# Kernel tuning notes

Hardware: AMD Instinct MI355X
Metric: run time of the kernel (lower is better)

The kernel has to match this reference:

```python
import jax, jax.numpy as jnp
import numpy as np

B, N, D = 2, 2048, 1024
CTX, TV = 256, 250
H, DH = 16, 64
INNER = H * DH          # 1024
FF = 4 * D              # 4096 (GEGLU inner)
SCALE = DH ** -0.5


def _layernorm(x, g, b):
    mu = x.mean(-1, keepdims=True)
    var = ((x - mu) ** 2).mean(-1, keepdims=True)
    return (x - mu) / jnp.sqrt(var + 1e-5) * g + b


def _attn(xq, ctx, wq, wk, wv, wo, bo):
    b, n, _ = xq.shape
    m = ctx.shape[1]
    q = (xq @ wq).reshape(b, n, H, DH)
    k = (ctx @ wk).reshape(b, m, H, DH)
    v = (ctx @ wv).reshape(b, m, H, DH)
    sim = jnp.einsum('bihd,bjhd->bhij', q, k) * SCALE
    att = jax.nn.softmax(sim, axis=-1)
    out = jnp.einsum('bhij,bjhd->bihd', att, v).reshape(b, n, INNER)
    return out @ wo + bo


def _sin_pe(T, d):
    pos = jnp.arange(T, dtype=jnp.float32)[:, None]
    den = jnp.power(10000.0, 2.0 * jnp.arange(d // 2, dtype=jnp.float32) / d)
    ang = pos / den                                  # [T, d/2]
    return jnp.stack([jnp.sin(ang), jnp.cos(ang)], -1).reshape(T, d)


def setup_inputs() -> dict:
    key = jax.random.key(0)
    ks = jax.random.split(key, 40)
    w = lambda k, s: jax.random.normal(k, s, jnp.float32) * 0.02
    inp = {
        'x': jax.random.normal(ks[0], (B, N, D), jnp.float32),
        'context': jax.random.normal(ks[1], (B, CTX, D), jnp.float32),
        'hint_control': jax.random.normal(ks[2], (B, TV, D), jnp.float32),
        'ln1_g': jnp.ones((D,)), 'ln1_b': jnp.zeros((D,)),
        'ln2_g': jnp.ones((D,)), 'ln2_b': jnp.zeros((D,)),
        'ln3_g': jnp.ones((D,)), 'ln3_b': jnp.zeros((D,)),
        'ln4_g': jnp.ones((D,)), 'ln4_b': jnp.zeros((D,)),
        'a1_wq': w(ks[3], (D, INNER)), 'a1_wk': w(ks[4], (D, INNER)),
        'a1_wv': w(ks[5], (D, INNER)), 'a1_wo': w(ks[6], (INNER, D)),
        'a1_bo': jnp.zeros((D,)),
        'a2_wq': w(ks[7], (D, INNER)), 'a2_wk': w(ks[8], (D, INNER)),
        'a2_wv': w(ks[9], (D, INNER)), 'a2_wo': w(ks[10], (INNER, D)),
        'a2_bo': jnp.zeros((D,)),
        'a3_wq': w(ks[11], (D, INNER)), 'a3_wk': w(ks[12], (D, INNER)),
        'a3_wv': w(ks[13], (D, INNER)), 'a3_wo': w(ks[14], (INNER, D)),
        'a3_bo': jnp.zeros((D,)),
        'ff_w1': w(ks[15], (D, 2 * FF)), 'ff_b1': jnp.zeros((2 * FF,)),
        'ff_w2': w(ks[16], (FF, D)), 'ff_b2': jnp.zeros((D,)),
    }
    return inp


def reference(x, context, hint_control,
              ln1_g, ln1_b, ln2_g, ln2_b, ln3_g, ln3_b, ln4_g, ln4_b,
              a1_wq, a1_wk, a1_wv, a1_wo, a1_bo,
              a2_wq, a2_wk, a2_wv, a2_wo, a2_bo,
              a3_wq, a3_wk, a3_wv, a3_wo, a3_bo,
              ff_w1, ff_b1, ff_w2, ff_b2):
    # attn1: self-attention (disable_self_attn=False -> context is x itself)
    h = _layernorm(x, ln1_g, ln1_b)
    x = _attn(h, h, a1_wq, a1_wk, a1_wv, a1_wo, a1_bo) + x
    # attn2: cross-attention over context
    h = _layernorm(x, ln2_g, ln2_b)
    x = _attn(h, context, a2_wq, a2_wk, a2_wv, a2_wo, a2_bo) + x
    # attn3: video cross-attention with sinusoidal PE added to hint_control
    hint = hint_control + _sin_pe(hint_control.shape[1], D)[None]
    h = _layernorm(x, ln4_g, ln4_b)
    x = _attn(h, hint, a3_wq, a3_wk, a3_wv, a3_wo, a3_bo) + x
    # GEGLU feed-forward
    h = _layernorm(x, ln3_g, ln3_b)
    proj = h @ ff_w1 + ff_b1
    a, gate = jnp.split(proj, 2, axis=-1)
    x = (a * jax.nn.gelu(gate, approximate=False)) @ ff_w2 + ff_b2 + x
    return x
```

## Files before the change

### kernel.cpp

```cpp
#include <hip/hip_runtime.h>
#include <cstdint>

typedef unsigned short u16;
typedef __bf16 bf16x8 __attribute__((ext_vector_type(8)));
typedef float f32x4 __attribute__((ext_vector_type(4)));

__device__ __forceinline__ u16 f2bf(float f) {
  union { float f; uint32_t u; } x; x.f = f;
  uint32_t r = x.u + 0x7FFFu + ((x.u >> 16) & 1u);
  return (u16)(r >> 16);
}
__device__ __forceinline__ bf16x8 ld8s(const u16* p) {
  return *reinterpret_cast<const bf16x8*>(p);
}
__device__ __forceinline__ float geluf(float x) {
  return 0.5f * x * (1.f + erff(x * 0.70710678118654752f));
}
__device__ __forceinline__ uint32_t cvtpk(float a, float b) {
  uint32_t r;
  asm("v_cvt_pk_bf16_f32 %0, %1, %2" : "=v"(r) : "v"(a), "v"(b));
  return r;
}
__device__ __forceinline__ void gload16(const u16* g, u16* l) {
  __builtin_amdgcn_global_load_lds(
      (__attribute__((address_space(1))) void*)const_cast<u16*>(g),
      (__attribute__((address_space(3))) void*)l, 16, 0, 0);
}

struct PrepJob {
  const void* src; void* dst;
  int K, N, mode, row_off, ldo, s_lo, s_hi, blk0;
};
struct PrepArgs { PrepJob j[17]; };

__global__ __launch_bounds__(256) void wprep_kernel(PrepArgs a) {
  __shared__ float tile[32][33];
  int bid = blockIdx.x;
  int t = threadIdx.x;
  const float* src = nullptr; void* dst = nullptr;
  int K = 0, N = 0, mode = 0, roff = 0, ldo = 0, slo = 0, shi = 0, bl = 0;
#pragma unroll
  for (int i = 0; i < 17; ++i) {
    int lo = a.j[i].blk0;
    int hi = (i == 16) ? 0x7fffffff : a.j[i + 1].blk0;
    if (bid >= lo && bid < hi) {
      src = (const float*)a.j[i].src; dst = a.j[i].dst;
      K = a.j[i].K; N = a.j[i].N; mode = a.j[i].mode; roff = a.j[i].row_off;
      ldo = a.j[i].ldo; slo = a.j[i].s_lo; shi = a.j[i].s_hi; bl = bid - lo;
    }
  }
  (void)K;
  if (mode <= 1) {
    int nb = N >> 5;
    int bx = bl % nb, by = bl / nb;
    int tx = t & 31, ty = t >> 5;
    int n = bx * 32 + tx, kbase = by * 32;
#pragma unroll
    for (int r = 0; r < 4; ++r)
      tile[ty + r * 8][tx] = src[(size_t)(kbase + ty + r * 8) * N + n];
    __syncthreads();
#pragma unroll
    for (int r = 0; r < 4; ++r) {
      int nl = ty + r * 8, ng = bx * 32 + nl;
      int orow;
      if (mode == 0) orow = roff + ng;
      else {
        if (ng < 4096) orow = ((ng >> 4) << 5) + (ng & 15);
        else { int t2 = ng - 4096; orow = ((t2 >> 4) << 5) + 16 + (t2 & 15); }
      }
      float v = tile[tx][nl];
      if (mode == 0 && orow >= slo && orow < shi) v *= 0.18033688011112042f;
      ((u16*)dst)[(size_t)orow * ldo + kbase + tx] = f2bf(v);
    }
  } else if (mode == 2) {
    int idx = bl * 1024 + t * 4;
    float4 v = *reinterpret_cast<const float4*>(src + idx);
    ushort4 o;
    o.x = f2bf(v.x); o.y = f2bf(v.y); o.z = f2bf(v.z); o.w = f2bf(v.w);
    *reinterpret_cast<ushort4*>((u16*)dst + idx) = o;
  } else if (mode == 3) {
    int row = bl;
    int tt = row % 250;
    int d0 = t * 4;
    int i0 = d0 >> 1;
    float den0 = powf(10000.f, (float)i0 / 512.f);
    float den1 = powf(10000.f, (float)(i0 + 1) / 512.f);
    float a0 = (float)tt / den0, a1 = (float)tt / den1;
    const float* hp = src + (size_t)row * 1024 + d0;
    u16* op = (u16*)dst + (size_t)row * 1024 + d0;
    op[0] = f2bf(hp[0] + sinf(a0));
    op[1] = f2bf(hp[1] + cosf(a0));
    op[2] = f2bf(hp[2] + sinf(a1));
    op[3] = f2bf(hp[3] + cosf(a1));
  } else {
    int i2 = bl * 256 + t;
    int g = i2 >> 5, s2 = i2 & 31;
    int c2 = (s2 < 16) ? (g * 16 + s2) : (4096 + g * 16 + (s2 - 16));
    ((float*)dst)[i2] = src[c2];
  }
}

__global__ __launch_bounds__(256) void ln_kernel(const float* __restrict__ x,
                                                 const float* __restrict__ g,
                                                 const float* __restrict__ b,
                                                 u16* __restrict__ out) {
  int row = blockIdx.x;
  int tid = threadIdx.x;
  int l = tid & 63, w = tid >> 6;
  const float4 v = reinterpret_cast<const float4*>(x + (size_t)row * 1024)[tid];
  float s = v.x + v.y + v.z + v.w;
#pragma unroll
  for (int d = 1; d < 64; d <<= 1) s += __shfl_xor(s, d, 64);
  __shared__ float red[8];
  if (l == 0) red[w] = s;
  __syncthreads();
  float mean = (red[0] + red[1] + red[2] + red[3]) * (1.f / 1024.f);
  float dx = v.x - mean, dy = v.y - mean, dz = v.z - mean, dw = v.w - mean;
  float vs = dx * dx + dy * dy + dz * dz + dw * dw;
#pragma unroll
  for (int d = 1; d < 64; d <<= 1) vs += __shfl_xor(vs, d, 64);
  if (l == 0) red[4 + w] = vs;
  __syncthreads();
  float var = (red[4] + red[5] + red[6] + red[7]) * (1.f / 1024.f);
  float rstd = rsqrtf(var + 1e-5f);
  const float4 g4 = reinterpret_cast<const float4*>(g)[tid];
  const float4 b4 = reinterpret_cast<const float4*>(b)[tid];
  ushort4 o;
  o.x = f2bf(dx * rstd * g4.x + b4.x);
  o.y = f2bf(dy * rstd * g4.y + b4.y);
  o.z = f2bf(dz * rstd * g4.z + b4.z);
  o.w = f2bf(dw * rstd * g4.w + b4.w);
  reinterpret_cast<ushort4*>(out + (size_t)row * 1024)[tid] = o;
}

template <int EPI>
__global__ __launch_bounds__(512, 2) void gemm256_kernel(
    const u16* __restrict__ A, int lda, const u16* __restrict__ Bt,
    void* __restrict__ Cv, int ldc, const float* __restrict__ bias,
    int M, int N, int K) {
  __shared__ __align__(16) u16 As[2][256 * 64];
  __shared__ __align__(16) u16 Bs[2][256 * 64];
  int t = threadIdx.x;
  int l = t & 63, w = t >> 6;
  int wm = w >> 2, wn = w & 3;
  int lr = l & 15, lg = l >> 4;
  int gx = gridDim.x;
  int nwg = gx * gridDim.y;
  int orig = blockIdx.y * gx + blockIdx.x;
  int qq = nwg >> 3, rr = nwg & 7;
  int xcd = orig & 7, lin = orig >> 3;
  int wg = (xcd < rr ? xcd * (qq + 1) : rr * (qq + 1) + (xcd - rr) * qq) + lin;
  int bx = wg % gx, by = wg / gx;
  int row0 = by * 256, n0 = bx * 256;

  int lrow8 = l >> 3, lchunk = l & 7;
  int csrc = (lchunk ^ lrow8) * 8;
  int keyA = lr & 7;

  f32x4 acc[8][4];
#pragma unroll
  for (int i = 0; i < 8; ++i)
#pragma unroll
    for (int j = 0; j < 4; ++j) acc[i][j] = f32x4{0.f, 0.f, 0.f, 0.f};

  auto stage = [&](int buf, int k0) {
#pragma unroll
    for (int q = 0; q < 4; ++q) {
      int rbase = w * 32 + q * 8;
      int r = rbase + lrow8;
      gload16(&A[(size_t)(row0 + r) * lda + k0 + csrc], &As[buf][rbase * 64]);
      gload16(&Bt[(size_t)(n0 + r) * K + k0 + csrc], &Bs[buf][rbase * 64]);
    }
  };

  int nk = K >> 6;
  stage(0, 0);
  if (nk > 1) {
    stage(1, 64);
    asm volatile("s_waitcnt vmcnt(8)" ::: "memory");
  } else {
    asm volatile("s_waitcnt vmcnt(0)" ::: "memory");
  }
  __builtin_amdgcn_sched_barrier(0);
  __builtin_amdgcn_s_barrier();
  int cur = 0;
  for (int ti = 0; ti < nk; ++ti) {
    __builtin_amdgcn_s_setprio(1);
#pragma unroll
    for (int kk = 0; kk < 2; ++kk) {
      int chunk = (((kk << 2) + lg) ^ keyA) << 3;
      bf16x8 af[8];
#pragma unroll
      for (int mi = 0; mi < 8; ++mi)
        af[mi] = ld8s(&As[cur][(wm * 128 + mi * 16 + lr) * 64 + chunk]);
      bf16x8 bfv[4];
#pragma unroll
      for (int ni = 0; ni < 4; ++ni)
        bfv[ni] = ld8s(&Bs[cur][(wn * 64 + ni * 16 + lr) * 64 + chunk]);
#pragma unroll
      for (int mi = 0; mi < 8; ++mi)
#pragma unroll
        for (int ni = 0; ni < 4; ++ni)
          acc[mi][ni] = __builtin_amdgcn_mfma_f32_16x16x32_bf16(af[mi], bfv[ni], acc[mi][ni], 0, 0, 0);
    }
    __builtin_amdgcn_s_setprio(0);
    __builtin_amdgcn_sched_barrier(0);
    __builtin_amdgcn_s_barrier();
    if (ti + 2 < nk) {
      stage(cur, (ti + 2) << 6);
      asm volatile("s_waitcnt vmcnt(8)" ::: "memory");
    } else {
      asm volatile("s_waitcnt vmcnt(0)" ::: "memory");
    }
    __builtin_amdgcn_sched_barrier(0);
    __builtin_amdgcn_s_barrier();
    cur ^= 1;
  }

#pragma unroll
  for (int mi = 0; mi < 8; ++mi) {
    int rowb = row0 + wm * 128 + mi * 16 + lg * 4;
    if (EPI == 2) {
#pragma unroll
      for (int p = 0; p < 2; ++p) {
        int colA = n0 + wn * 64 + p * 32 + lr;
        int colG = colA + 16;
        int ocol = ((n0 + wn * 64) >> 1) + p * 16 + lr;
#pragma unroll
        for (int r = 0; r < 4; ++r) {
          float av = acc[mi][2 * p][r] + bias[colA];
          float gv = acc[mi][2 * p + 1][r] + bias[colG];
          ((u16*)Cv)[(size_t)(rowb + r) * ldc + ocol] = f2bf(av * geluf(gv));
        }
      }
    } else {
#pragma unroll
      for (int ni = 0; ni < 4; ++ni) {
        int gcol = n0 + wn * 64 + ni * 16 + lr;
#pragma unroll
        for (int r = 0; r < 4; ++r)
          ((u16*)Cv)[(size_t)(rowb + r) * ldc + gcol] = f2bf(acc[mi][ni][r]);
      }
    }
  }
}

template <int EPI, bool GUARD>
__global__ __launch_bounds__(256) void gemm_bt_kernel(
    const u16* __restrict__ A, int lda, const u16* __restrict__ Bt,
    void* __restrict__ Cv, int ldc, const float* __restrict__ bias,
    const float* __restrict__ res, int M, int N, int K) {
  __shared__ __align__(16) u16 As[2][128 * 64];
  __shared__ __align__(16) u16 Bs[2][128 * 64];
  int t = threadIdx.x;
  int l = t & 63, w = t >> 6;
  int wm = w >> 1, wn = w & 1;
  int lr = l & 15, lg = l >> 4;
  int gx = gridDim.x;
  int nwg = gx * gridDim.y;
  int orig = blockIdx.y * gx + blockIdx.x;
  int qq = nwg >> 3, rr = nwg & 7;
  int xcd = orig & 7, lin = orig >> 3;
  int wg = (xcd < rr ? xcd * (qq + 1) : rr * (qq + 1) + (xcd - rr) * qq) + lin;
  int bx = wg % gx, by = wg / gx;
  int row0 = by * 128, n0 = bx * 128;

  int lrow8 = l >> 3, lchunk = l & 7;
  int csrc = (lchunk ^ lrow8) * 8;
  int keyA = lr & 7;
  f32x4 acc[4][4];
#pragma unroll
  for (int i = 0; i < 4; ++i)
#pragma unroll
    for (int j = 0; j < 4; ++j) acc[i][j] = f32x4{0.f, 0.f, 0.f, 0.f};

  auto stage = [&](int buf, int k0) {
#pragma unroll
    for (int q = 0; q < 4; ++q) {
      int rbase = w * 32 + q * 8;
      int r = rbase + lrow8;
      int ga = row0 + r;
      if (GUARD) { if (ga > M - 1) ga = M - 1; }
      gload16(&A[(size_t)ga * lda + k0 + csrc], &As[buf][rbase * 64]);
      gload16(&Bt[(size_t)(n0 + r) * K + k0 + csrc], &Bs[buf][rbase * 64]);
    }
  };

  int nk = K >> 6;
  stage(0, 0);
  if (nk > 1) {
    stage(1, 64);
    asm volatile("s_waitcnt vmcnt(8)" ::: "memory");
  } else {
    asm volatile("s_waitcnt vmcnt(0)" ::: "memory");
  }
  __builtin_amdgcn_sched_barrier(0);
  __builtin_amdgcn_s_barrier();
  int cur = 0;
  for (int ti = 0; ti < nk; ++ti) {
    __builtin_amdgcn_s_setprio(1);
#pragma unroll
    for (int kk = 0; kk < 2; ++kk) {
      bf16x8 af[4], bfv[4];
#pragma unroll
      for (int mi = 0; mi < 4; ++mi)
        af[mi] = ld8s(&As[cur][(wm * 64 + mi * 16 + lr) * 64 + ((((kk << 2) + lg) ^ keyA) << 3)]);
#pragma unroll
      for (int ni = 0; ni < 4; ++ni)
        bfv[ni] = ld8s(&Bs[cur][(wn * 64 + ni * 16 + lr) * 64 + ((((kk << 2) + lg) ^ keyA) << 3)]);
#pragma unroll
      for (int mi = 0; mi < 4; ++mi)
#pragma unroll
        for (int ni = 0; ni < 4; ++ni)
          acc[mi][ni] = __builtin_amdgcn_mfma_f32_16x16x32_bf16(af[mi], bfv[ni], acc[mi][ni], 0, 0, 0);
    }
    __builtin_amdgcn_s_setprio(0);
    __builtin_amdgcn_sched_barrier(0);
    __builtin_amdgcn_s_barrier();
    if (ti + 2 < nk) {
      stage(cur, (ti + 2) << 6);
      asm volatile("s_waitcnt vmcnt(8)" ::: "memory");
    } else {
      asm volatile("s_waitcnt vmcnt(0)" ::: "memory");
    }
    __builtin_amdgcn_sched_barrier(0);
    __builtin_amdgcn_s_barrier();
    cur ^= 1;
  }

#pragma unroll
  for (int mi = 0; mi < 4; ++mi) {
    int rowb = row0 + wm * 64 + mi * 16 + lg * 4;
    if (EPI == 2) {
#pragma unroll
      for (int p = 0; p < 2; ++p) {
        int colA = n0 + wn * 64 + p * 32 + lr;
        int colG = colA + 16;
        int ocol = ((n0 + wn * 64) >> 1) + p * 16 + lr;
#pragma unroll
        for (int r = 0; r < 4; ++r) {
          int grow = rowb + r;
          float av = acc[mi][2 * p][r] + bias[colA];
          float gv = acc[mi][2 * p + 1][r] + bias[colG];
          ((u16*)Cv)[(size_t)grow * ldc + ocol] = f2bf(av * geluf(gv));
        }
      }
    } else {
#pragma unroll
      for (int ni = 0; ni < 4; ++ni) {
        int gcol = n0 + wn * 64 + ni * 16 + lr;
#pragma unroll
        for (int r = 0; r < 4; ++r) {
          int grow = rowb + r;
          if (GUARD && grow >= M) continue;
          float v = acc[mi][ni][r];
          if (EPI == 0)
            ((u16*)Cv)[(size_t)grow * ldc + gcol] = f2bf(v);
          else
            ((float*)Cv)[(size_t)grow * ldc + gcol] =
                v + bias[gcol] + res[(size_t)grow * ldc + gcol];
        }
      }
    }
  }
}

template <bool TG>
__global__ __launch_bounds__(256) void attn_kernel(
    const u16* __restrict__ Q, int qs, int qoff,
    const u16* __restrict__ KV, int kvs, int koff, int voff,
    int m, u16* __restrict__ O) {
  int b = blockIdx.z, h = blockIdx.y;
  int t = threadIdx.x;
  int l = t & 63, w = t >> 6;
  int lr = l & 15, lg = l >> 4;
  int q0 = blockIdx.x * 128 + w * 16;
  __shared__ __align__(16) u16 Ks[2][64 * 64];
  __shared__ __align__(16) u16 Vt[2][64 * 64];
  __shared__ __align__(16) u16 Pl[4][16 * 64];

  const u16* qrowA = Q + (size_t)((b << 11) + q0 + lr) * qs + qoff + h * 64;
  const u16* qrowB = qrowA + (size_t)64 * qs;
  bf16x8 qa0 = ld8s(qrowA + lg * 8), qa1 = ld8s(qrowA + 32 + lg * 8);
  bf16x8 qb0 = ld8s(qrowB + lg * 8), qb1 = ld8s(qrowB + 32 + lg * 8);

  f32x4 oA[4], oB[4];
  float psA = 0.f, psB = 0.f;
#pragma unroll
  for (int r = 0; r < 4; ++r) { oA[r] = f32x4{0.f, 0.f, 0.f, 0.f}; oB[r] = f32x4{0.f, 0.f, 0.f, 0.f}; }

  const u16* kvb = KV + (size_t)b * m * kvs + h * 64;
  int kj = t >> 3, kc = t & 7;
  int srcsw = ((l & 7) ^ (l >> 3)) << 3;
  int psw = (lr & 7) ^ ((lr & 8) >> 1);

  {
#pragma unroll
    for (int q2 = 0; q2 < 2; ++q2) {
      int gr = w * 16 + q2 * 8 + (l >> 3);
      if (TG) { if (gr > m - 1) gr = m - 1; }
      gload16(kvb + (size_t)gr * kvs + koff + srcsw, &Ks[0][(w * 16 + q2 * 8) * 64]);
    }
    int jv = kj * 2;
    int gv0 = jv, gv1 = jv + 1;
    if (TG) { if (gv0 > m - 1) gv0 = m - 1; if (gv1 > m - 1) gv1 = m - 1; }
    uint4 va = *reinterpret_cast<const uint4*>(kvb + (size_t)gv0 * kvs + voff + kc * 8);
    uint4 vb2 = *reinterpret_cast<const uint4*>(kvb + (size_t)gv1 * kvs + voff + kc * 8);
    const u16* vap = reinterpret_cast<const u16*>(&va);
    const u16* vbp = reinterpret_cast<const u16*>(&vb2);
    int jb = jv >> 3, jlow = jv & 7;
#pragma unroll
    for (int i = 0; i < 8; ++i) {
      int d = kc * 8 + i;
      int key = (d ^ (d >> 3)) & 7;
      uint32_t pk = (uint32_t)vap[i] | ((uint32_t)vbp[i] << 16);
      *reinterpret_cast<uint32_t*>(&Vt[0][d * 64 + ((jb ^ key) << 3) + jlow]) = pk;
    }
  }
  __syncthreads();

  int nj = (m + 63) >> 6;
  int cur = 0;
  for (int jt = 0; jt < nj; ++jt) {
    int j0 = jt << 6;
    bool hn = (jt + 1 < nj);
    uint4 va, vb2;
    if (hn) {
      int j0n = j0 + 64;
#pragma unroll
      for (int q2 = 0; q2 < 2; ++q2) {
        int gr = j0n + w * 16 + q2 * 8 + (l >> 3);
        if (TG) { if (gr > m - 1) gr = m - 1; }
        gload16(kvb + (size_t)gr * kvs + koff + srcsw, &Ks[cur ^ 1][(w * 16 + q2 * 8) * 64]);
      }
      int jv = kj * 2;
      int gv0 = j0n + jv, gv1 = j0n + jv + 1;
      if (TG) { if (gv0 > m - 1) gv0 = m - 1; if (gv1 > m - 1) gv1 = m - 1; }
      va = *reinterpret_cast<const uint4*>(kvb + (size_t)gv0 * kvs + voff + kc * 8);
      vb2 = *reinterpret_cast<const uint4*>(kvb + (size_t)gv1 * kvs + voff + kc * 8);
    }

    const u16* Kb = Ks[cur];
    f32x4 sA[4], sB[4];
#pragma unroll
    for (int c = 0; c < 4; ++c) {
      sA[c] = f32x4{0.f, 0.f, 0.f, 0.f};
      sB[c] = f32x4{0.f, 0.f, 0.f, 0.f};
      bf16x8 k0 = ld8s(&Kb[(c * 16 + lr) * 64 + ((lg ^ (lr & 7)) << 3)]);
      bf16x8 k1 = ld8s(&Kb[(c * 16 + lr) * 64 + (((4 + lg) ^ (lr & 7)) << 3)]);
      sA[c] = __builtin_amdgcn_mfma_f32_16x16x32_bf16(k0, qa0, sA[c], 0, 0, 0);
      sA[c] = __builtin_amdgcn_mfma_f32_16x16x32_bf16(k1, qa1, sA[c], 0, 0, 0);
      sB[c] = __builtin_amdgcn_mfma_f32_16x16x32_bf16(k0, qb0, sB[c], 0, 0, 0);
      sB[c] = __builtin_amdgcn_mfma_f32_16x16x32_bf16(k1, qb1, sB[c], 0, 0, 0);
    }

    if (hn) {
      const u16* vap = reinterpret_cast<const u16*>(&va);
      const u16* vbp = reinterpret_cast<const u16*>(&vb2);
      int jv = kj * 2;
      int jb = jv >> 3, jlow = jv & 7;
#pragma unroll
      for (int i = 0; i < 8; ++i) {
        int d = kc * 8 + i;
        int key = (d ^ (d >> 3)) & 7;
        uint32_t pk = (uint32_t)vap[i] | ((uint32_t)vbp[i] << 16);
        *reinterpret_cast<uint32_t*>(&Vt[cur ^ 1][d * 64 + ((jb ^ key) << 3) + jlow]) = pk;
      }
    }

    bool tail = TG && (j0 + 64 > m);
    const u16* Vb = Vt[cur];
    bf16x8 vfr[2][4];

    {
      uint32_t pk[8];
#pragma unroll
      for (int c = 0; c < 4; ++c) {
        float p[4];
#pragma unroll
        for (int r = 0; r < 4; ++r) {
          float v = exp2f(sA[c][r]);
          if (tail && (j0 + c * 16 + lg * 4 + r >= m)) v = 0.f;
          p[r] = v; psA += v;
        }
        pk[2 * c] = cvtpk(p[0], p[1]);
        pk[2 * c + 1] = cvtpk(p[2], p[3]);
      }
#pragma unroll
      for (int c = 0; c < 4; ++c) {
        int phys = (2 * c + (lg >> 1)) ^ psw;
        uint2 u; u.x = pk[2 * c]; u.y = pk[2 * c + 1];
        *reinterpret_cast<uint2*>(&Pl[w][lr * 64 + (phys << 3) + ((lg & 1) << 2)]) = u;
      }
#pragma unroll
      for (int ks = 0; ks < 2; ++ks) {
        int physp = (ks * 4 + lg) ^ psw;
        bf16x8 pb = ld8s(&Pl[w][lr * 64 + (physp << 3)]);
#pragma unroll
        for (int dt = 0; dt < 4; ++dt) {
          int d = dt * 16 + lr;
          int key = (d ^ (d >> 3)) & 7;
          vfr[ks][dt] = ld8s(&Vb[d * 64 + ((((ks << 2) + lg) ^ key) << 3)]);
          oA[dt] = __builtin_amdgcn_mfma_f32_16x16x32_bf16(vfr[ks][dt], pb, oA[dt], 0, 0, 0);
        }
      }
    }
    {
      uint32_t pk[8];
#pragma unroll
      for (int c = 0; c < 4; ++c) {
        float p[4];
#pragma unroll
        for (int r = 0; r < 4; ++r) {
          float v = exp2f(sB[c][r]);
          if (tail && (j0 + c * 16 + lg * 4 + r >= m)) v = 0.f;
          p[r] = v; psB += v;
        }
        pk[2 * c] = cvtpk(p[0], p[1]);
        pk[2 * c + 1] = cvtpk(p[2], p[3]);
      }
#pragma unroll
      for (int c = 0; c < 4; ++c) {
        int phys = (2 * c + (lg >> 1)) ^ psw;
        uint2 u; u.x = pk[2 * c]; u.y = pk[2 * c + 1];
        *reinterpret_cast<uint2*>(&Pl[w][lr * 64 + (phys << 3) + ((lg & 1) << 2)]) = u;
      }
#pragma unroll
      for (int ks = 0; ks < 2; ++ks) {
        int physp = (ks * 4 + lg) ^ psw;
        bf16x8 pb = ld8s(&Pl[w][lr * 64 + (physp << 3)]);
#pragma unroll
        for (int dt = 0; dt < 4; ++dt)
          oB[dt] = __builtin_amdgcn_mfma_f32_16x16x32_bf16(vfr[ks][dt], pb, oB[dt], 0, 0, 0);
      }
    }
    __syncthreads();
    cur ^= 1;
  }

  psA += __shfl_xor(psA, 16, 64); psA += __shfl_xor(psA, 32, 64);
  psB += __shfl_xor(psB, 16, 64); psB += __shfl_xor(psB, 32, 64);
  float invA = 1.f / psA, invB = 1.f / psB;
  {
    int grow = (b << 11) + q0 + lr;
    u16* op = O + (size_t)grow * 1024 + h * 64 + lg * 4;
#pragma unroll
    for (int dt = 0; dt < 4; ++dt) {
      uint2 u;
      u.x = cvtpk(oA[dt][0] * invA, oA[dt][1] * invA);
      u.y = cvtpk(oA[dt][2] * invA, oA[dt][3] * invA);
      *reinterpret_cast<uint2*>(op + dt * 16) = u;
    }
    u16* op2 = op + (size_t)64 * 1024;
#pragma unroll
    for (int dt = 0; dt < 4; ++dt) {
      uint2 u;
      u.x = cvtpk(oB[dt][0] * invB, oB[dt][1] * invB);
      u.y = cvtpk(oB[dt][2] * invB, oB[dt][3] * invB);
      *reinterpret_cast<uint2*>(op2 + dt * 16) = u;
    }
  }
}

extern "C" void kernel_launch(void* const* d_in, const int* in_sizes, int n_in,
                              void* d_out, int out_size, void* d_ws, size_t ws_size,
                              hipStream_t stream) {
  const float* x_in = (const float*)d_in[0];
  const float* ctx_in = (const float*)d_in[1];
  const float* hint_in = (const float*)d_in[2];
  const float* ln1g = (const float*)d_in[3]; const float* ln1b = (const float*)d_in[4];
  const float* ln2g = (const float*)d_in[5]; const float* ln2b = (const float*)d_in[6];
  const float* ln3g = (const float*)d_in[7]; const float* ln3b = (const float*)d_in[8];
  const float* ln4g = (const float*)d_in[9]; const float* ln4b = (const float*)d_in[10];
  const float* a1wq = (const float*)d_in[11]; const float* a1wk = (const float*)d_in[12];
  const float* a1wv = (const float*)d_in[13]; const float* a1wo = (const float*)d_in[14];
  const float* a1bo = (const float*)d_in[15];
  const float* a2wq = (const float*)d_in[16]; const float* a2wk = (const float*)d_in[17];
  const float* a2wv = (const float*)d_in[18]; const float* a2wo = (const float*)d_in[19];
  const float* a2bo = (const float*)d_in[20];
  const float* a3wq = (const float*)d_in[21]; const float* a3wk = (const float*)d_in[22];
  const float* a3wv = (const float*)d_in[23]; const float* a3wo = (const float*)d_in[24];
  const float* a3bo = (const float*)d_in[25];
  const float* ffw1 = (const float*)d_in[26]; const float* ffb1 = (const float*)d_in[27];
  const float* ffw2 = (const float*)d_in[28]; const float* ffb2 = (const float*)d_in[29];

  char* wsb = (char*)d_ws;
  size_t off = 0;
  auto alloc = [&](size_t bytes) -> void* {
    void* p = wsb + off;
    off += (bytes + 255) & ~(size_t)255;
    return p;
  };
  u16* wqkv1t = (u16*)alloc(3072ull * 1024 * 2);
  u16* wo1t = (u16*)alloc(1024ull * 1024 * 2);
  u16* wq2t = (u16*)alloc(1024ull * 1024 * 2);
  u16* wkv2t = (u16*)alloc(2048ull * 1024 * 2);
  u16* wo2t = (u16*)alloc(1024ull * 1024 * 2);
  u16* wq3t = (u16*)alloc(1024ull * 1024 * 2);
  u16* wkv3t = (u16*)alloc(2048ull * 1024 * 2);
  u16* wo3t = (u16*)alloc(1024ull * 1024 * 2);
  u16* w1t = (u16*)alloc(8192ull * 1024 * 2);
  u16* w2t = (u16*)alloc(1024ull * 4096 * 2);
  float* b1p = (float*)alloc(8192ull * 4);
  u16* hintbf = (u16*)alloc(500ull * 1024 * 2);
  u16* ctxbf = (u16*)alloc(512ull * 1024 * 2);
  float* xbuf = (float*)alloc(4096ull * 1024 * 4);
  u16* hbf = (u16*)alloc(4096ull * 1024 * 2);
  u16* attnout = (u16*)alloc(4096ull * 1024 * 2);
  u16* qbuf = (u16*)alloc(4096ull * 1024 * 2);
  u16* kvbuf = (u16*)alloc(512ull * 2048 * 2);
  u16* qkv = (u16*)alloc(4096ull * 4096 * 2);
  u16* gbuf = qkv;

  PrepArgs pa;
  int bi = 0, bc = 0;
  auto addJ = [&](const void* s, void* d, int K, int N, int mode, int roff,
                  int ldo, int slo, int shi, int nblk) {
    pa.j[bi].src = s; pa.j[bi].dst = d; pa.j[bi].K = K; pa.j[bi].N = N;
    pa.j[bi].mode = mode; pa.j[bi].row_off = roff; pa.j[bi].ldo = ldo;
    pa.j[bi].s_lo = slo; pa.j[bi].s_hi = shi; pa.j[bi].blk0 = bc;
    bc += nblk; ++bi;
  };
  addJ(a1wq, wqkv1t, 1024, 1024, 0, 0, 1024, 0, 1024, 1024);
  addJ(a1wk, wqkv1t, 1024, 1024, 0, 1024, 1024, 0, 0, 1024);
  addJ(a1wv, wqkv1t, 1024, 1024, 0, 2048, 1024, 0, 0, 1024);
  addJ(a1wo, wo1t, 1024, 1024, 0, 0, 1024, 0, 0, 1024);
  addJ(a2wq, wq2t, 1024, 1024, 0, 0, 1024, 0, 1024, 1024);
  addJ(a2wk, wkv2t, 1024, 1024, 0, 0, 1024, 0, 0, 1024);
  addJ(a2wv, wkv2t, 1024, 1024, 0, 1024, 1024, 0, 0, 1024);
  addJ(a2wo, wo2t, 1024, 1024, 0, 0, 1024, 0, 0, 1024);
  addJ(a3wq, wq3t, 1024, 1024, 0, 0, 1024, 0, 1024, 1024);
  addJ(a3wk, wkv3t, 1024, 1024, 0, 0, 1024, 0, 0, 1024);
  addJ(a3wv, wkv3t, 1024, 1024, 0, 1024, 1024, 0, 0, 1024);
  addJ(a3wo, wo3t, 1024, 1024, 0, 0, 1024, 0, 0, 1024);
  addJ(ffw1, w1t, 1024, 8192, 1, 0, 1024, 0, 0, 8192);
  addJ(ffw2, w2t, 4096, 1024, 0, 0, 4096, 0, 0, 4096);
  addJ(ctx_in, ctxbf, 0, 0, 2, 0, 0, 0, 0, 512);
  addJ(hint_in, hintbf, 0, 0, 3, 0, 0, 0, 0, 500);
  addJ(ffb1, b1p, 0, 0, 4, 0, 0, 0, 0, 32);
  wprep_kernel<<<bc, 256, 0, stream>>>(pa);

  ln_kernel<<<4096, 256, 0, stream>>>(x_in, ln1g, ln1b, hbf);
  gemm256_kernel<0><<<dim3(12, 16), 512, 0, stream>>>(hbf, 1024, wqkv1t, qkv, 3072,
                                                      nullptr, 4096, 3072, 1024);
  attn_kernel<false><<<dim3(16, 16, 2), 256, 0, stream>>>(qkv, 3072, 0, qkv, 3072, 1024, 2048,
                                                          2048, attnout);
  gemm_bt_kernel<1, false><<<dim3(8, 32), 256, 0, stream>>>(attnout, 1024, wo1t, xbuf, 1024,
                                                            a1bo, x_in, 4096, 1024, 1024);

  ln_kernel<<<4096, 256, 0, stream>>>(xbuf, ln2g, ln2b, hbf);
  gemm_bt_kernel<0, false><<<dim3(8, 32), 256, 0, stream>>>(hbf, 1024, wq2t, qbuf, 1024,
                                                            nullptr, nullptr, 4096, 1024, 1024);
  gemm_bt_kernel<0, false><<<dim3(16, 4), 256, 0, stream>>>(ctxbf, 1024, wkv2t, kvbuf, 2048,
                                                            nullptr, nullptr, 512, 2048, 1024);
  attn_kernel<false><<<dim3(16, 16, 2), 256, 0, stream>>>(qbuf, 1024, 0, kvbuf, 2048, 0, 1024,
                                                          256, attnout);
  gemm_bt_kernel<1, false><<<dim3(8, 32), 256, 0, stream>>>(attnout, 1024, wo2t, xbuf, 1024,
                                                            a2bo, xbuf, 4096, 1024, 1024);

  ln_kernel<<<4096, 256, 0, stream>>>(xbuf, ln4g, ln4b, hbf);
  gemm_bt_kernel<0, false><<<dim3(8, 32), 256, 0, stream>>>(hbf, 1024, wq3t, qbuf, 1024,
                                                            nullptr, nullptr, 4096, 1024, 1024);
  gemm_bt_kernel<0, true><<<dim3(16, 4), 256, 0, stream>>>(hintbf, 1024, wkv3t, kvbuf, 2048,
                                                           nullptr, nullptr, 500, 2048, 1024);
  attn_kernel<true><<<dim3(16, 16, 2), 256, 0, stream>>>(qbuf, 1024, 0, kvbuf, 2048, 0, 1024,
                                                         250, attnout);
  gemm_bt_kernel<1, false><<<dim3(8, 32), 256, 0, stream>>>(attnout, 1024, wo3t, xbuf, 1024,
                                                            a3bo, xbuf, 4096, 1024, 1024);

  ln_kernel<<<4096, 256, 0, stream>>>(xbuf, ln3g, ln3b, hbf);
  gemm256_kernel<2><<<dim3(32, 16), 512, 0, stream>>>(hbf, 1024, w1t, gbuf, 4096,
                                                      b1p, 4096, 8192, 1024);
  gemm_bt_kernel<1, false><<<dim3(8, 32), 256, 0, stream>>>(gbuf, 4096, w2t, d_out, 1024,
                                                            ffb2, xbuf, 4096, 1024, 4096);
}
```

Baseline: 508.1 us.

## Interleave next-tile global loads with split MFMA phases in 256x256 GEMM

Restructures the 256x256 bf16 GEMM main loop from a prefetch-two-ahead double buffer into a one-ahead schedule. Each K tile is split into four sub-phases of LDS reads plus 16 MFMAs, and the next tile's A and B global-to-LDS loads are spread across those phases with barriers between them. The aim is to overlap memory traffic with compute more finely and cut register pressure from holding eight A fragments at once. The trade-off is more s_barrier synchronisation per tile, less prefetch distance, and a delicate vmcnt and buffer-reuse ordering.

```diff
diff --git a/kernel.cpp b/kernel.cpp
--- a/kernel.cpp
+++ b/kernel.cpp
@@ -155,7 +155,9 @@
 
   int lrow8 = l >> 3, lchunk = l & 7;
   int csrc = (lchunk ^ lrow8) * 8;
-  int keyA = lr & 7;
+  int keyA = lr & 15 & 7;
+  int c0 = ((lg ^ keyA) << 3);
+  int c1 = (((4 + lg) ^ keyA) << 3);
 
   f32x4 acc[8][4];
 #pragma unroll
@@ -163,58 +165,90 @@
 #pragma unroll
     for (int j = 0; j < 4; ++j) acc[i][j] = f32x4{0.f, 0.f, 0.f, 0.f};
 
-  auto stage = [&](int buf, int k0) {
-#pragma unroll
-    for (int q = 0; q < 4; ++q) {
-      int rbase = w * 32 + q * 8;
-      int r = rbase + lrow8;
-      gload16(&A[(size_t)(row0 + r) * lda + k0 + csrc], &As[buf][rbase * 64]);
-      gload16(&Bt[(size_t)(n0 + r) * K + k0 + csrc], &Bs[buf][rbase * 64]);
-    }
+  auto stA = [&](int buf, int k0, int q) {
+    int rb = q * 64 + w * 8;
+    gload16(&A[(size_t)(row0 + rb + lrow8) * lda + k0 + csrc], &As[buf][rb * 64]);
   };
+  auto stB = [&](int buf, int k0, int q) {
+    int rb = q * 64 + w * 8;
+    gload16(&Bt[(size_t)(n0 + rb + lrow8) * K + k0 + csrc], &Bs[buf][rb * 64]);
+  };
 
   int nk = K >> 6;
-  stage(0, 0);
-  if (nk > 1) {
-    stage(1, 64);
-    asm volatile("s_waitcnt vmcnt(8)" ::: "memory");
-  } else {
-    asm volatile("s_waitcnt vmcnt(0)" ::: "memory");
-  }
+  stB(0, 0, 0); stB(0, 0, 1); stB(0, 0, 2); stB(0, 0, 3);
+  stA(0, 0, 0); stA(0, 0, 2); stA(0, 0, 1); stA(0, 0, 3);
+  asm volatile("s_waitcnt vmcnt(2)" ::: "memory");
   __builtin_amdgcn_sched_barrier(0);
-  __builtin_amdgcn_s_barrier();
-  int cur = 0;
+  asm volatile("s_barrier" ::: "memory");
+
   for (int ti = 0; ti < nk; ++ti) {
+    int cur = ti & 1, nxt = cur ^ 1;
+    bool hn = (ti + 1 < nk);
+    int k0n = (ti + 1) << 6;
+    const u16* Ab = As[cur];
+    const u16* Bb = Bs[cur];
+    bf16x8 a[4], b[4];
+
+#pragma unroll
+    for (int mi = 0; mi < 4; ++mi) a[mi] = ld8s(&Ab[(wm * 128 + mi * 16 + lr) * 64 + c0]);
+#pragma unroll
+    for (int ni = 0; ni < 4; ++ni) b[ni] = ld8s(&Bb[(wn * 64 + ni * 16 + lr) * 64 + c0]);
+    if (hn) { stB(nxt, k0n, 0); stB(nxt, k0n, 1); }
+    asm volatile("s_barrier" ::: "memory");
     __builtin_amdgcn_s_setprio(1);
 #pragma unroll
-    for (int kk = 0; kk < 2; ++kk) {
-      int chunk = (((kk << 2) + lg) ^ keyA) << 3;
-      bf16x8 af[8];
-#pragma unroll
-      for (int mi = 0; mi < 8; ++mi)
-        af[mi] = ld8s(&As[cur][(wm * 128 + mi * 16 + lr) * 64 + chunk]);
-      bf16x8 bfv[4];
+    for (int mi = 0; mi < 4; ++mi)
 #pragma unroll
       for (int ni = 0; ni < 4; ++ni)
-        bfv[ni] = ld8s(&Bs[cur][(wn * 64 + ni * 16 + lr) * 64 + chunk]);
-#pragma unroll
-      for (int mi = 0; mi < 8; ++mi)
-#pragma unroll
-        for (int ni = 0; ni < 4; ++ni)
-          acc[mi][ni] = __builtin_amdgcn_mfma_f32_16x16x32_bf16(af[mi], bfv[ni], acc[mi][ni], 0, 0, 0);
-    }
+        acc[mi][ni] = __builtin_amdgcn_mfma_f32_16x16x32_bf16(a[mi], b[ni], acc[mi][ni], 0, 0, 0);
     __builtin_amdgcn_s_setprio(0);
+    if (hn) asm volatile("s_waitcnt vmcnt(2)" ::: "memory");
+    else    asm volatile("s_waitcnt vmcnt(0)" ::: "memory");
     __builtin_amdgcn_sched_barrier(0);
-    __builtin_amdgcn_s_barrier();
-    if (ti + 2 < nk) {
-      stage(cur, (ti + 2) << 6);
-      asm volatile("s_waitcnt vmcnt(8)" ::: "memory");
-    } else {
-      asm volatile("s_waitcnt vmcnt(0)" ::: "memory");
-    }
+    asm volatile("s_barrier" ::: "memory");
+
+#pragma unroll
+    for (int mi = 0; mi < 4; ++mi) a[mi] = ld8s(&Ab[(wm * 128 + (mi + 4) * 16 + lr) * 64 + c0]);
+    if (hn) { stB(nxt, k0n, 2); stB(nxt, k0n, 3); }
+    asm volatile("s_barrier" ::: "memory");
+    __builtin_amdgcn_s_setprio(1);
+#pragma unroll
+    for (int mi = 0; mi < 4; ++mi)
+#pragma unroll
+      for (int ni = 0; ni < 4; ++ni)
+        acc[mi + 4][ni] = __builtin_amdgcn_mfma_f32_16x16x32_bf16(a[mi], b[ni], acc[mi + 4][ni], 0, 0, 0);
+    __builtin_amdgcn_s_setprio(0);
+    asm volatile("s_barrier" ::: "memory");
+
+#pragma unroll
+    for (int mi = 0; mi < 4; ++mi) a[mi] = ld8s(&Ab[(wm * 128 + mi * 16 + lr) * 64 + c1]);
+#pragma unroll
+    for (int ni = 0; ni < 4; ++ni) b[ni] = ld8s(&Bb[(wn * 64 + ni * 16 + lr) * 64 + c1]);
+    if (hn) { stA(nxt, k0n, 0); stA(nxt, k0n, 2); }
+    asm volatile("s_barrier" ::: "memory");
+    __builtin_amdgcn_s_setprio(1);
+#pragma unroll
+    for (int mi = 0; mi < 4; ++mi)
+#pragma unroll
+      for (int ni = 0; ni < 4; ++ni)
+        acc[mi][ni] = __builtin_amdgcn_mfma_f32_16x16x32_bf16(a[mi], b[ni], acc[mi][ni], 0, 0, 0);
+    __builtin_amdgcn_s_setprio(0);
+    asm volatile("s_barrier" ::: "memory");
+
+#pragma unroll
+    for (int mi = 0; mi < 4; ++mi) a[mi] = ld8s(&Ab[(wm * 128 + (mi + 4) * 16 + lr) * 64 + c1]);
+    if (hn) { stA(nxt, k0n, 1); stA(nxt, k0n, 3); }
+    asm volatile("s_barrier" ::: "memory");
+    __builtin_amdgcn_s_setprio(1);
+#pragma unroll
+    for (int mi = 0; mi < 4; ++mi)
+#pragma unroll
+      for (int ni = 0; ni < 4; ++ni)
+        acc[mi + 4][ni] = __builtin_amdgcn_mfma_f32_16x16x32_bf16(a[mi], b[ni], acc[mi + 4][ni], 0, 0, 0);
+    __builtin_amdgcn_s_setprio(0);
+    if (hn) asm volatile("s_waitcnt vmcnt(2)" ::: "memory");
     __builtin_amdgcn_sched_barrier(0);
-    __builtin_amdgcn_s_barrier();
-    cur ^= 1;
+    asm volatile("s_barrier" ::: "memory");
   }
 
 #pragma unroll
```

New measurement: 499.1 us. No clear change (-1.8%).
